# Kernel tuning notes

Hardware: AMD Instinct MI355X
Metric: run time of the kernel (lower is better)

## Reference

```python
import jax, jax.numpy as jnp
import numpy as np

B, L = 512, 8192          # batch, document length
N = 128                   # output_sentence_num
S = 256                   # output_sentence_len
DELIM = 5                 # delimiter token
PAD = 0                   # pad_word
CUT_HEAD = False
VOCAB = 100


def setup_inputs() -> dict:
    key = jax.random.key(0)
    x = jax.random.randint(key, (B, L), 0, VOCAB, dtype=jnp.int32)
    return {"x": x}


def reference(x):
    b, l = x.shape
    # right-padded row: original tokens + one trailing delimiter, shape [B, L+1]
    rpad = jnp.concatenate([x, jnp.full((b, 1), DELIM, x.dtype)], axis=1)
    # segment id of rpad position j = number of delimiters in x[:j]
    cum = jnp.cumsum((x == DELIM).astype(jnp.int32), axis=1)           # [B, L]
    seg = jnp.concatenate([jnp.zeros((b, 1), jnp.int32), cum], axis=1)  # [B, L+1]
    seg = jnp.minimum(seg, N - 1)  # segments >= N-1 merged into last chunk (tail merge)
    j = jnp.arange(l + 1, dtype=jnp.int32)
    bidx = jnp.arange(b)[:, None]
    # start index of each segment (min j with seg==k); unused segments stay at L+1
    starts = jnp.full((b, N), l + 1, jnp.int32)
    starts = starts.at[bidx, seg].min(jnp.broadcast_to(j, (b, l + 1)))
    pos = j[None, :] - jnp.take_along_axis(starts, seg, axis=1)  # offset within chunk
    # chunk sizes (number of rpad positions per segment)
    sizes = jnp.zeros((b, N), jnp.int32).at[bidx, seg].add(jnp.ones((b, l + 1), jnp.int32))
    size_here = jnp.take_along_axis(sizes, seg, axis=1)
    # size-1 chunks (lone delimiter == empty sentence) are filled with pad_word
    vals = jnp.where(size_here == 1, jnp.int32(PAD), rpad)
    if CUT_HEAD:
        p = pos - 1
        valid = (pos >= 1) & (pos <= S - 1)  # chunk[1:S], then padded to S
    else:
        p = pos
        valid = pos <= S - 1                 # chunk[:S]
    # scatter into [B, N, S]; invalid positions routed out-of-bounds and dropped
    k_idx = jnp.where(valid, seg, N)
    p_idx = jnp.where(valid, p, S)
    otp = jnp.full((b, N, S), PAD, x.dtype)
    otp = otp.at[bidx, k_idx, p_idx].set(vals, mode='drop')
    # lengths / mask (tf.count_nonzero semantics; pad_word == 0)
    len_sent = jnp.sum((otp != 0).astype(jnp.int32), axis=2)   # [B, N]
    len_doc = jnp.sum((len_sent != 0).astype(jnp.int32), axis=1)  # [B]
    mask = (jnp.arange(S)[None, None, :] < len_sent[..., None]).astype(jnp.float32)
    return otp, len_doc, mask
```

## Files before the change

kernel.cpp:

```cpp
#include <hip/hip_runtime.h>

#define B_ 512
#define L_ 8192
#define N_ 128
#define S_ 256
#define DELIM_ 5
#define T_ 1024
#define NW_ (T_ / 64)

__global__ __launch_bounds__(T_, 8) void split_kernel(const int* __restrict__ x,
                                                      float* __restrict__ otp,
                                                      float* __restrict__ len_doc,
                                                      float* __restrict__ mask) {
    const int b = blockIdx.x;
    const int t = threadIdx.x;
    const int lane = t & 63;
    const int w = t >> 6;
    const int* __restrict__ row = x + (size_t)b * L_;

    __shared__ int s_wsum[NW_];
    __shared__ int s_dpos[N_ - 1];
    __shared__ int s_doc[NW_];

    const int4 r0 = ((const int4*)row)[t];
    const int4 r1 = ((const int4*)row)[t + T_];

    const int c0 = (r0.x == DELIM_) + (r0.y == DELIM_) + (r0.z == DELIM_) + (r0.w == DELIM_);
    const int c1 = (r1.x == DELIM_) + (r1.y == DELIM_) + (r1.z == DELIM_) + (r1.w == DELIM_);
    const int packed = c0 | (c1 << 16);

    int sv = packed;
#pragma unroll
    for (int d = 1; d < 64; d <<= 1) {
        int n = __shfl_up(sv, d, 64);
        if (lane >= d) sv += n;
    }
    if (lane == 63) s_wsum[w] = sv;
    __syncthreads();

    int woff = 0, tot = 0;
#pragma unroll
    for (int i = 0; i < NW_; ++i) {
        const int s = s_wsum[i];
        if (i < w) woff += s;
        tot += s;
    }
    const int pre = woff + sv - packed;
    const int c0tot = tot & 0xffff;
    const int m = c0tot + (tot >> 16);
    const int off0 = pre & 0xffff;
    const int off1 = c0tot + (pre >> 16);

    if (c0 > 0 && off0 < N_ - 1) {
        int o = off0;
        const int p = 4 * t;
        if (r0.x == DELIM_) { if (o < N_ - 1) s_dpos[o] = p;     ++o; }
        if (r0.y == DELIM_) { if (o < N_ - 1) s_dpos[o] = p + 1; ++o; }
        if (r0.z == DELIM_) { if (o < N_ - 1) s_dpos[o] = p + 2; ++o; }
        if (r0.w == DELIM_) { if (o < N_ - 1) s_dpos[o] = p + 3; ++o; }
    }
    if (c1 > 0 && off1 < N_ - 1) {
        int o = off1;
        const int p = 4 * T_ + 4 * t;
        if (r1.x == DELIM_) { if (o < N_ - 1) s_dpos[o] = p;     ++o; }
        if (r1.y == DELIM_) { if (o < N_ - 1) s_dpos[o] = p + 1; ++o; }
        if (r1.z == DELIM_) { if (o < N_ - 1) s_dpos[o] = p + 2; ++o; }
        if (r1.w == DELIM_) { if (o < N_ - 1) s_dpos[o] = p + 3; ++o; }
    }
    __syncthreads();

    const int mc = (m < N_ - 1) ? m : (N_ - 1);
    float* __restrict__ otp_b = otp + (size_t)b * N_ * S_;
    float* __restrict__ msk_b = mask + (size_t)b * N_ * S_;
    int doccnt = 0;
#pragma unroll
    for (int i = 0; i < (N_ / NW_); ++i) {
        const int k = i * NW_ + w;
        int cl = 0, start = 0;
        if (k <= mc) {
            start = (k == 0) ? 0 : (s_dpos[k - 1] + 1);
            const int end = (k < mc) ? s_dpos[k] : L_;
            const int size = end - start + 1;
            cl = (size <= 1) ? 0 : (size < S_ ? size : S_);
        }
        int t0 = 0, t1 = 0, t2 = 0, t3 = 0;
        int len = 0;
        if (cl > 0) {
            {
                const int idx = start + lane;
                int v0 = row[idx < L_ ? idx : L_ - 1];
                v0 = (idx == L_) ? DELIM_ : v0;
                t0 = (lane < cl) ? v0 : 0;
            }
            {
                const int idx = start + 64 + lane;
                int v1 = row[idx < L_ ? idx : L_ - 1];
                v1 = (idx == L_) ? DELIM_ : v1;
                t1 = (64 + lane < cl) ? v1 : 0;
            }
            {
                const int idx = start + 128 + lane;
                int v2 = row[idx < L_ ? idx : L_ - 1];
                v2 = (idx == L_) ? DELIM_ : v2;
                t2 = (128 + lane < cl) ? v2 : 0;
            }
            {
                const int idx = start + 192 + lane;
                int v3 = row[idx < L_ ? idx : L_ - 1];
                v3 = (idx == L_) ? DELIM_ : v3;
                t3 = (192 + lane < cl) ? v3 : 0;
            }
            len += __popcll(__ballot(t0 != 0));
            len += __popcll(__ballot(t1 != 0));
            len += __popcll(__ballot(t2 != 0));
            len += __popcll(__ballot(t3 != 0));
        }
        otp_b[(size_t)k * S_ + lane]       = (float)t0;
        otp_b[(size_t)k * S_ + lane + 64]  = (float)t1;
        otp_b[(size_t)k * S_ + lane + 128] = (float)t2;
        otp_b[(size_t)k * S_ + lane + 192] = (float)t3;
        msk_b[(size_t)k * S_ + lane]       = (lane       < len) ? 1.0f : 0.0f;
        msk_b[(size_t)k * S_ + lane + 64]  = (lane + 64  < len) ? 1.0f : 0.0f;
        msk_b[(size_t)k * S_ + lane + 128] = (lane + 128 < len) ? 1.0f : 0.0f;
        msk_b[(size_t)k * S_ + lane + 192] = (lane + 192 < len) ? 1.0f : 0.0f;
        doccnt += (len > 0);
    }

    if (lane == 0) s_doc[w] = doccnt;
    __syncthreads();
    if (t == 0) {
        int d = 0;
#pragma unroll
        for (int i = 0; i < NW_; ++i) d += s_doc[i];
        len_doc[b] = (float)d;
    }
}

extern "C" void kernel_launch(void* const* d_in, const int* in_sizes, int n_in,
                              void* d_out, int out_size, void* d_ws, size_t ws_size,
                              hipStream_t stream) {
    const int* x = (const int*)d_in[0];
    float* out = (float*)d_out;

    float* otp = out;
    float* len_doc = out + (size_t)B_ * N_ * S_;
    float* mask = len_doc + B_;

    split_kernel<<<B_, T_, 0, stream>>>(x, otp, len_doc, mask);
}
```

Measured before the change: 141.9 us.

## Split into table-building kernel and grid-stride vectorized write kernel

Splits the single per-row kernel into two. The first computes per-sentence start, clipped length and nonzero count into a workspace table, plus len_doc. The second is a persistent grid-stride kernel that writes otp and mask with 16-byte vector stores, one wave per sentence. The aim is to spread the large output-write traffic over more blocks and use wider stores instead of 1024-thread blocks per row. In exchange it adds a second launch, a round trip through the table, and re-reads of input tokens. It falls back to the old kernel when the workspace is too small.

```diff
diff --git a/kernel.cpp b/kernel.cpp
--- a/kernel.cpp
+++ b/kernel.cpp
@@ -7,6 +7,156 @@
 #define DELIM_ 5
 #define T_ 1024
 #define NW_ (T_ / 64)
+#define TW_ 256
+#define GW_ 2048
+
+typedef float __attribute__((ext_vector_type(4))) f32x4;
+
+__global__ __launch_bounds__(T_) void table_kernel(const int* __restrict__ x,
+                                                   int4* __restrict__ tbl,
+                                                   float* __restrict__ len_doc) {
+    const int b = blockIdx.x;
+    const int t = threadIdx.x;
+    const int lane = t & 63;
+    const int w = t >> 6;
+    const int* __restrict__ row = x + (size_t)b * L_;
+
+    __shared__ int s_wsum[NW_];
+    __shared__ int s_dpos[N_ - 1];
+    __shared__ int s_start[N_];
+    __shared__ int s_cl[N_];
+    __shared__ int s_doc[NW_];
+
+    const int4 r0 = ((const int4*)row)[t];
+    const int4 r1 = ((const int4*)row)[t + T_];
+
+    const int c0 = (r0.x == DELIM_) + (r0.y == DELIM_) + (r0.z == DELIM_) + (r0.w == DELIM_);
+    const int c1 = (r1.x == DELIM_) + (r1.y == DELIM_) + (r1.z == DELIM_) + (r1.w == DELIM_);
+    const int packed = c0 | (c1 << 16);
+
+    int sv = packed;
+#pragma unroll
+    for (int d = 1; d < 64; d <<= 1) {
+        int n = __shfl_up(sv, d, 64);
+        if (lane >= d) sv += n;
+    }
+    if (lane == 63) s_wsum[w] = sv;
+    __syncthreads();
+
+    int woff = 0, tot = 0;
+#pragma unroll
+    for (int i = 0; i < NW_; ++i) {
+        const int s = s_wsum[i];
+        if (i < w) woff += s;
+        tot += s;
+    }
+    const int pre = woff + sv - packed;
+    const int c0tot = tot & 0xffff;
+    const int m = c0tot + (tot >> 16);
+    const int off0 = pre & 0xffff;
+    const int off1 = c0tot + (pre >> 16);
+
+    if (c0 > 0 && off0 < N_ - 1) {
+        int o = off0;
+        const int p = 4 * t;
+        if (r0.x == DELIM_) { if (o < N_ - 1) s_dpos[o] = p;     ++o; }
+        if (r0.y == DELIM_) { if (o < N_ - 1) s_dpos[o] = p + 1; ++o; }
+        if (r0.z == DELIM_) { if (o < N_ - 1) s_dpos[o] = p + 2; ++o; }
+        if (r0.w == DELIM_) { if (o < N_ - 1) s_dpos[o] = p + 3; ++o; }
+    }
+    if (c1 > 0 && off1 < N_ - 1) {
+        int o = off1;
+        const int p = 4 * T_ + 4 * t;
+        if (r1.x == DELIM_) { if (o < N_ - 1) s_dpos[o] = p;     ++o; }
+        if (r1.y == DELIM_) { if (o < N_ - 1) s_dpos[o] = p + 1; ++o; }
+        if (r1.z == DELIM_) { if (o < N_ - 1) s_dpos[o] = p + 2; ++o; }
+        if (r1.w == DELIM_) { if (o < N_ - 1) s_dpos[o] = p + 3; ++o; }
+    }
+    __syncthreads();
+
+    if (t < N_) {
+        const int k = t;
+        const int mc = (m < N_ - 1) ? m : (N_ - 1);
+        int start = 0, cl = 0;
+        if (k <= mc) {
+            start = (k == 0) ? 0 : (s_dpos[k - 1] + 1);
+            const int end = (k < mc) ? s_dpos[k] : L_;
+            const int size = end - start + 1;
+            cl = (size <= 1) ? 0 : (size < S_ ? size : S_);
+        }
+        s_start[k] = start;
+        s_cl[k] = cl;
+    }
+    __syncthreads();
+
+    int doccnt = 0;
+#pragma unroll
+    for (int i = 0; i < (N_ / NW_); ++i) {
+        const int k = i * NW_ + w;
+        const int start = s_start[k];
+        const int cl = s_cl[k];
+        int len = 0;
+        if (cl > 0) {
+#pragma unroll
+            for (int j = 0; j < 4; ++j) {
+                const int e = 64 * j + lane;
+                const int idx = start + e;
+                int v = row[idx < L_ ? idx : L_ - 1];
+                v = (idx == L_) ? DELIM_ : v;
+                v = (e < cl) ? v : 0;
+                len += __popcll(__ballot(v != 0));
+            }
+        }
+        doccnt += (len > 0);
+        if (lane == 0) tbl[b * N_ + k] = make_int4(start, cl, len, 0);
+    }
+
+    if (lane == 0) s_doc[w] = doccnt;
+    __syncthreads();
+    if (t == 0) {
+        int d = 0;
+#pragma unroll
+        for (int i = 0; i < NW_; ++i) d += s_doc[i];
+        len_doc[b] = (float)d;
+    }
+}
+
+__global__ __launch_bounds__(TW_, 8) void write_kernel(const int* __restrict__ x,
+                                                       const int4* __restrict__ tbl,
+                                                       float* __restrict__ otp,
+                                                       float* __restrict__ mask) {
+    const int lane = threadIdx.x & 63;
+    const int wid = (blockIdx.x * TW_ + threadIdx.x) >> 6;
+    const int nw = (GW_ * TW_) >> 6;
+    const int e0 = lane << 2;
+
+    for (int s = wid; s < B_ * N_; s += nw) {
+        const int4 tc = tbl[s];
+        const int start = tc.x, cl = tc.y, len = tc.z;
+
+        f32x4 mk;
+        mk.x = (e0 + 0 < len) ? 1.0f : 0.0f;
+        mk.y = (e0 + 1 < len) ? 1.0f : 0.0f;
+        mk.z = (e0 + 2 < len) ? 1.0f : 0.0f;
+        mk.w = (e0 + 3 < len) ? 1.0f : 0.0f;
+        *(f32x4*)(mask + (size_t)s * S_ + e0) = mk;
+
+        f32x4 tf = {0.f, 0.f, 0.f, 0.f};
+        if (cl > 0) {
+            const int b = s >> 7;
+            const int* __restrict__ row = x + (size_t)b * L_;
+#pragma unroll
+            for (int j = 0; j < 4; ++j) {
+                const int e = e0 + j;
+                const int idx = start + e;
+                int v = row[idx < L_ ? idx : L_ - 1];
+                v = (idx == L_) ? DELIM_ : v;
+                if (e < cl) tf[j] = (float)v;
+            }
+        }
+        *(f32x4*)(otp + (size_t)s * S_ + e0) = tf;
+    }
+}
 
 __global__ __launch_bounds__(T_, 8) void split_kernel(const int* __restrict__ x,
                                                       float* __restrict__ otp,
@@ -86,30 +236,10 @@
         int t0 = 0, t1 = 0, t2 = 0, t3 = 0;
         int len = 0;
         if (cl > 0) {
-            {
-                const int idx = start + lane;
-                int v0 = row[idx < L_ ? idx : L_ - 1];
-                v0 = (idx == L_) ? DELIM_ : v0;
-                t0 = (lane < cl) ? v0 : 0;
-            }
-            {
-                const int idx = start + 64 + lane;
-                int v1 = row[idx < L_ ? idx : L_ - 1];
-                v1 = (idx == L_) ? DELIM_ : v1;
-                t1 = (64 + lane < cl) ? v1 : 0;
-            }
-            {
-                const int idx = start + 128 + lane;
-                int v2 = row[idx < L_ ? idx : L_ - 1];
-                v2 = (idx == L_) ? DELIM_ : v2;
-                t2 = (128 + lane < cl) ? v2 : 0;
-            }
-            {
-                const int idx = start + 192 + lane;
-                int v3 = row[idx < L_ ? idx : L_ - 1];
-                v3 = (idx == L_) ? DELIM_ : v3;
-                t3 = (192 + lane < cl) ? v3 : 0;
-            }
+            { const int idx = start + lane;       int v = row[idx < L_ ? idx : L_ - 1]; v = (idx == L_) ? DELIM_ : v; t0 = (lane < cl) ? v : 0; }
+            { const int idx = start + 64 + lane;  int v = row[idx < L_ ? idx : L_ - 1]; v = (idx == L_) ? DELIM_ : v; t1 = (64 + lane < cl) ? v : 0; }
+            { const int idx = start + 128 + lane; int v = row[idx < L_ ? idx : L_ - 1]; v = (idx == L_) ? DELIM_ : v; t2 = (128 + lane < cl) ? v : 0; }
+            { const int idx = start + 192 + lane; int v = row[idx < L_ ? idx : L_ - 1]; v = (idx == L_) ? DELIM_ : v; t3 = (192 + lane < cl) ? v : 0; }
             len += __popcll(__ballot(t0 != 0));
             len += __popcll(__ballot(t1 != 0));
             len += __popcll(__ballot(t2 != 0));
@@ -146,5 +276,12 @@
     float* len_doc = out + (size_t)B_ * N_ * S_;
     float* mask = len_doc + B_;
 
-    split_kernel<<<B_, T_, 0, stream>>>(x, otp, len_doc, mask);
-}
+    const size_t tbl_bytes = (size_t)B_ * N_ * sizeof(int4);
+    if (d_ws != nullptr && ws_size >= tbl_bytes) {
+        int4* tbl = (int4*)d_ws;
+        table_kernel<<<B_, T_, 0, stream>>>(x, tbl, len_doc);
+        write_kernel<<<GW_, TW_, 0, stream>>>(x, tbl, otp, mask);
+    } else {
+        split_kernel<<<B_, T_, 0, stream>>>(x, otp, len_doc, mask);
+    }
+}
```

Result: slower. 150.4 us (+6.0%).
